# Optimization experiments

Measured on AMD Instinct MI355X. Metric: run time of the kernel, lower is better.

The kernel has to match this reference:

```python
import jax, jax.numpy as jnp
import numpy as np

DIM = 100   # hardcoded in the original module (A_100.npy / target_100.npy)
BATCH = 131072
B_COEF = 1.0  # self.B in the original module


def setup_inputs() -> dict:
    key = jax.random.key(0)
    k1, k2, k3 = jax.random.split(key, 3)
    # state layout per system: [x (DIM), e_x (DIM), W_c (DIM), W_a (DIM)]
    state = jax.random.normal(k1, (BATCH, 4 * DIM), dtype=jnp.float32)
    A = jax.random.normal(k2, (DIM, DIM), dtype=jnp.float32) / np.sqrt(DIM)
    target = jax.random.normal(k3, (DIM,), dtype=jnp.float32)
    return {"state": state, "A": A, "target": target}


def reference(state, A, target):
    # Faithful, batched translation of CA_event.forward(t, state):
    #   x, e_x, W_a are slices of the flattened 4*DIM state; W_c is unused in forward.
    d = DIM
    x = state[:, :d]            # [B, d]
    e_x = state[:, d:2 * d]     # [B, d]
    W_a = state[:, 3 * d:4 * d]  # [B, d]

    u = W_a * (x + e_x - target[None, :])          # control signal
    s = x * x / (1.0 + x * x)                      # sigmoid-like saturation Y^2/(1+Y^2)
    dx = -B_COEF * x + s @ A.T + u * s             # [B, d]

    zeros = jnp.zeros_like(x)
    # derivative ordering matches the original output tuple: (dx, -dx, 0 for W_c, 0 for W_a)
    return jnp.concatenate([dx, -dx, zeros, zeros], axis=-1)
```

## Files before the change

kernel.cpp:

```cpp
#include <hip/hip_runtime.h>

#define DIMX 100
#define BATCH 131072
#define DXW 104

typedef __bf16 bf16x8 __attribute__((ext_vector_type(8)));
typedef float  f32x4  __attribute__((ext_vector_type(4)));

__global__ void conv_A(const float* __restrict__ A, __bf16* __restrict__ ws) {
    int i = blockIdx.x * 256 + threadIdx.x;
    if (i < 112 * 128) {
        int j = i >> 7, k = i & 127;
        float v = (j < DIMX && k < DIMX) ? A[j * DIMX + k] : 0.0f;
        ws[i] = (__bf16)v;
    }
}

template <bool USE_WS>
__global__ __launch_bounds__(128) void ca_main(
    const float* __restrict__ state, const float* __restrict__ Amat,
    const __bf16* __restrict__ Bws, const float* __restrict__ target,
    float* __restrict__ out)
{
    __shared__ __align__(16) float dxbuf[2][16 * DXW];

    const int tid = threadIdx.x;
    const int wave = tid >> 6, lane = tid & 63;
    float* __restrict__ wbuf = dxbuf[wave];
    const int fr = lane & 15, h = lane >> 4;
    const long r0 = (long)blockIdx.x * 32 + wave * 16;
    const float* rp = state + (r0 + fr) * 400;

    bf16x8 sfrag[4];
#pragma unroll
    for (int kt = 0; kt < 4; ++kt) {
        int k0 = kt * 32 + h * 8;
        bf16x8 f = {};
        if (k0 < DIMX) {
            f32x4 xa = *reinterpret_cast<const f32x4*>(rp + k0);
            f32x4 xb = *reinterpret_cast<const f32x4*>(rp + k0 + 4);
#pragma unroll
            for (int e = 0; e < 8; ++e) {
                float x = (e < 4) ? xa[e] : xb[e - 4];
                float x2 = x * x;
                float s = x2 * __builtin_amdgcn_rcpf(1.0f + x2);
                f[e] = (k0 + e < DIMX) ? (__bf16)s : (__bf16)0.0f;
            }
        }
        sfrag[kt] = f;
    }

#pragma unroll
    for (int n = 0; n < 7; ++n) {
        f32x4 acc = {0.f, 0.f, 0.f, 0.f};
#pragma unroll
        for (int kt = 0; kt < 4; ++kt) {
            bf16x8 af;
            if constexpr (USE_WS) {
                af = *reinterpret_cast<const bf16x8*>(
                    Bws + (n * 16 + fr) * 128 + kt * 32 + h * 8);
            } else {
                int jj = n * 16 + fr;
#pragma unroll
                for (int e = 0; e < 8; ++e) {
                    int k = kt * 32 + h * 8 + e;
                    float v = (jj < DIMX && k < DIMX) ? Amat[jj * DIMX + k] : 0.0f;
                    af[e] = (__bf16)v;
                }
            }
            acc = __builtin_amdgcn_mfma_f32_16x16x32_bf16(af, sfrag[kt], acc, 0, 0, 0);
        }
        int j0 = n * 16 + h * 4;
        if (j0 < DIMX) {
            f32x4 x = *reinterpret_cast<const f32x4*>(rp + j0);
            f32x4 e = *reinterpret_cast<const f32x4*>(rp + DIMX + j0);
            f32x4 w = *reinterpret_cast<const f32x4*>(rp + 3 * DIMX + j0);
            f32x4 t = *reinterpret_cast<const f32x4*>(target + j0);
            f32x4 dx;
#pragma unroll
            for (int q = 0; q < 4; ++q) {
                float u  = w[q] * (x[q] + e[q] - t[q]);
                float x2 = x[q] * x[q];
                float s  = x2 * __builtin_amdgcn_rcpf(1.0f + x2);
                dx[q] = acc[q] + fmaf(u, s, -x[q]);
            }
            *reinterpret_cast<f32x4*>(&wbuf[fr * DXW + j0]) = dx;
        }
    }

#pragma unroll
    for (int it = 0; it < 25; ++it) {
        int i = lane + it * 64;
        int row = i / 100, c4 = i - row * 100;
        f32x4 v;
        if (c4 < 25) {
            v = *reinterpret_cast<const f32x4*>(&wbuf[row * DXW + c4 * 4]);
        } else if (c4 < 50) {
            f32x4 d = *reinterpret_cast<const f32x4*>(&wbuf[row * DXW + (c4 - 25) * 4]);
            v = f32x4{-d[0], -d[1], -d[2], -d[3]};
        } else {
            v = f32x4{0.f, 0.f, 0.f, 0.f};
        }
        __builtin_nontemporal_store(v,
            reinterpret_cast<f32x4*>(&out[(r0 + row) * 400 + c4 * 4]));
    }
}

extern "C" void kernel_launch(void* const* d_in, const int* in_sizes, int n_in,
                              void* d_out, int out_size, void* d_ws, size_t ws_size,
                              hipStream_t stream) {
    const float* state  = (const float*)d_in[0];
    const float* Amat   = (const float*)d_in[1];
    const float* target = (const float*)d_in[2];
    float* out = (float*)d_out;
    (void)in_sizes; (void)n_in; (void)out_size;

    if (ws_size >= (size_t)(112 * 128 * sizeof(__bf16))) {
        conv_A<<<dim3(56), dim3(256), 0, stream>>>(Amat, (__bf16*)d_ws);
        ca_main<true><<<dim3(BATCH / 32), dim3(128), 0, stream>>>(
            state, Amat, (const __bf16*)d_ws, target, out);
    } else {
        ca_main<false><<<dim3(BATCH / 32), dim3(128), 0, stream>>>(
            state, Amat, nullptr, target, out);
    }
}
```

Measured before the change: 71.60 us.

## Make main kernel persistent with grid-stride tiles and register prefetch of next x

```diff
diff --git a/kernel.cpp b/kernel.cpp
--- a/kernel.cpp
+++ b/kernel.cpp
@@ -2,7 +2,9 @@
 
 #define DIMX 100
 #define BATCH 131072
-#define DXW 104
+#define DXW 100
+#define NTILES (BATCH / 16)
+#define GRID 1024
 
 typedef __bf16 bf16x8 __attribute__((ext_vector_type(8)));
 typedef float  f32x4  __attribute__((ext_vector_type(4)));
@@ -28,81 +30,110 @@
     const int wave = tid >> 6, lane = tid & 63;
     float* __restrict__ wbuf = dxbuf[wave];
     const int fr = lane & 15, h = lane >> 4;
-    const long r0 = (long)blockIdx.x * 32 + wave * 16;
-    const float* rp = state + (r0 + fr) * 400;
+    const int wstride = GRID * 2;
+    const int wid = blockIdx.x * 2 + wave;
 
-    bf16x8 sfrag[4];
-#pragma unroll
-    for (int kt = 0; kt < 4; ++kt) {
-        int k0 = kt * 32 + h * 8;
-        bf16x8 f = {};
-        if (k0 < DIMX) {
-            f32x4 xa = *reinterpret_cast<const f32x4*>(rp + k0);
-            f32x4 xb = *reinterpret_cast<const f32x4*>(rp + k0 + 4);
-#pragma unroll
-            for (int e = 0; e < 8; ++e) {
-                float x = (e < 4) ? xa[e] : xb[e - 4];
-                float x2 = x * x;
-                float s = x2 * __builtin_amdgcn_rcpf(1.0f + x2);
-                f[e] = (k0 + e < DIMX) ? (__bf16)s : (__bf16)0.0f;
-            }
-        }
-        sfrag[kt] = f;
-    }
-
-#pragma unroll
-    for (int n = 0; n < 7; ++n) {
-        f32x4 acc = {0.f, 0.f, 0.f, 0.f};
+    f32x4 RA[4], RB[4];
+    {
+        const float* rp0 = state + ((long)wid * 16 + fr) * 400;
 #pragma unroll
         for (int kt = 0; kt < 4; ++kt) {
-            bf16x8 af;
-            if constexpr (USE_WS) {
-                af = *reinterpret_cast<const bf16x8*>(
-                    Bws + (n * 16 + fr) * 128 + kt * 32 + h * 8);
-            } else {
-                int jj = n * 16 + fr;
-#pragma unroll
-                for (int e = 0; e < 8; ++e) {
-                    int k = kt * 32 + h * 8 + e;
-                    float v = (jj < DIMX && k < DIMX) ? Amat[jj * DIMX + k] : 0.0f;
-                    af[e] = (__bf16)v;
-                }
+            int k0 = kt * 32 + h * 8;
+            if (k0 < DIMX) {
+                RA[kt] = *reinterpret_cast<const f32x4*>(rp0 + k0);
+                RB[kt] = *reinterpret_cast<const f32x4*>(rp0 + k0 + 4);
             }
-            acc = __builtin_amdgcn_mfma_f32_16x16x32_bf16(af, sfrag[kt], acc, 0, 0, 0);
-        }
-        int j0 = n * 16 + h * 4;
-        if (j0 < DIMX) {
-            f32x4 x = *reinterpret_cast<const f32x4*>(rp + j0);
-            f32x4 e = *reinterpret_cast<const f32x4*>(rp + DIMX + j0);
-            f32x4 w = *reinterpret_cast<const f32x4*>(rp + 3 * DIMX + j0);
-            f32x4 t = *reinterpret_cast<const f32x4*>(target + j0);
-            f32x4 dx;
-#pragma unroll
-            for (int q = 0; q < 4; ++q) {
-                float u  = w[q] * (x[q] + e[q] - t[q]);
-                float x2 = x[q] * x[q];
-                float s  = x2 * __builtin_amdgcn_rcpf(1.0f + x2);
-                dx[q] = acc[q] + fmaf(u, s, -x[q]);
-            }
-            *reinterpret_cast<f32x4*>(&wbuf[fr * DXW + j0]) = dx;
         }
     }
 
+    for (int t = wid; t < NTILES; t += wstride) {
+        const long r0 = (long)t * 16;
+        const float* rp = state + (r0 + fr) * 400;
+
+        bf16x8 sfrag[4];
 #pragma unroll
-    for (int it = 0; it < 25; ++it) {
-        int i = lane + it * 64;
-        int row = i / 100, c4 = i - row * 100;
-        f32x4 v;
-        if (c4 < 25) {
-            v = *reinterpret_cast<const f32x4*>(&wbuf[row * DXW + c4 * 4]);
-        } else if (c4 < 50) {
-            f32x4 d = *reinterpret_cast<const f32x4*>(&wbuf[row * DXW + (c4 - 25) * 4]);
-            v = f32x4{-d[0], -d[1], -d[2], -d[3]};
-        } else {
-            v = f32x4{0.f, 0.f, 0.f, 0.f};
+        for (int kt = 0; kt < 4; ++kt) {
+            int k0 = kt * 32 + h * 8;
+            bf16x8 f = {};
+            if (k0 < DIMX) {
+#pragma unroll
+                for (int e = 0; e < 8; ++e) {
+                    float x = (e < 4) ? RA[kt][e] : RB[kt][e - 4];
+                    float x2 = x * x;
+                    float s = x2 * __builtin_amdgcn_rcpf(1.0f + x2);
+                    f[e] = (k0 + e < DIMX) ? (__bf16)s : (__bf16)0.0f;
+                }
+            }
+            sfrag[kt] = f;
         }
-        __builtin_nontemporal_store(v,
-            reinterpret_cast<f32x4*>(&out[(r0 + row) * 400 + c4 * 4]));
+
+        int tn = t + wstride;
+        if (tn < NTILES) {
+            const float* rpn = state + ((long)tn * 16 + fr) * 400;
+#pragma unroll
+            for (int kt = 0; kt < 4; ++kt) {
+                int k0 = kt * 32 + h * 8;
+                if (k0 < DIMX) {
+                    RA[kt] = *reinterpret_cast<const f32x4*>(rpn + k0);
+                    RB[kt] = *reinterpret_cast<const f32x4*>(rpn + k0 + 4);
+                }
+            }
+        }
+
+#pragma unroll
+        for (int n = 0; n < 7; ++n) {
+            f32x4 acc = {0.f, 0.f, 0.f, 0.f};
+#pragma unroll
+            for (int kt = 0; kt < 4; ++kt) {
+                bf16x8 af;
+                if constexpr (USE_WS) {
+                    af = *reinterpret_cast<const bf16x8*>(
+                        Bws + (n * 16 + fr) * 128 + kt * 32 + h * 8);
+                } else {
+                    int jj = n * 16 + fr;
+#pragma unroll
+                    for (int e = 0; e < 8; ++e) {
+                        int k = kt * 32 + h * 8 + e;
+                        float v = (jj < DIMX && k < DIMX) ? Amat[jj * DIMX + k] : 0.0f;
+                        af[e] = (__bf16)v;
+                    }
+                }
+                acc = __builtin_amdgcn_mfma_f32_16x16x32_bf16(af, sfrag[kt], acc, 0, 0, 0);
+            }
+            int j0 = n * 16 + h * 4;
+            if (j0 < DIMX) {
+                f32x4 x = *reinterpret_cast<const f32x4*>(rp + j0);
+                f32x4 e = *reinterpret_cast<const f32x4*>(rp + DIMX + j0);
+                f32x4 w = *reinterpret_cast<const f32x4*>(rp + 3 * DIMX + j0);
+                f32x4 tt = *reinterpret_cast<const f32x4*>(target + j0);
+                f32x4 dx;
+#pragma unroll
+                for (int q = 0; q < 4; ++q) {
+                    float u  = w[q] * (x[q] + e[q] - tt[q]);
+                    float x2 = x[q] * x[q];
+                    float s  = x2 * __builtin_amdgcn_rcpf(1.0f + x2);
+                    dx[q] = acc[q] + fmaf(u, s, -x[q]);
+                }
+                *reinterpret_cast<f32x4*>(&wbuf[fr * DXW + j0]) = dx;
+            }
+        }
+
+#pragma unroll
+        for (int it = 0; it < 25; ++it) {
+            int i = lane + it * 64;
+            int row = i / 100, c4 = i - row * 100;
+            f32x4 v;
+            if (c4 < 25) {
+                v = *reinterpret_cast<const f32x4*>(&wbuf[row * DXW + c4 * 4]);
+            } else if (c4 < 50) {
+                f32x4 d = *reinterpret_cast<const f32x4*>(&wbuf[row * DXW + (c4 - 25) * 4]);
+                v = f32x4{-d[0], -d[1], -d[2], -d[3]};
+            } else {
+                v = f32x4{0.f, 0.f, 0.f, 0.f};
+            }
+            __builtin_nontemporal_store(v,
+                reinterpret_cast<f32x4*>(&out[(r0 + row) * 400 + c4 * 4]));
+        }
     }
 }
 
@@ -117,10 +148,10 @@
 
     if (ws_size >= (size_t)(112 * 128 * sizeof(__bf16))) {
         conv_A<<<dim3(56), dim3(256), 0, stream>>>(Amat, (__bf16*)d_ws);
-        ca_main<true><<<dim3(BATCH / 32), dim3(128), 0, stream>>>(
+        ca_main<true><<<dim3(GRID), dim3(128), 0, stream>>>(
             state, Amat, (const __bf16*)d_ws, target, out);
     } else {
-        ca_main<false><<<dim3(BATCH / 32), dim3(128), 0, stream>>>(
+        ca_main<false><<<dim3(GRID), dim3(128), 0, stream>>>(
             state, Amat, nullptr, target, out);
     }
 }
```

Result: slower. 79.30 us (+10.8%).
